# Performance work log

Measured on AMD Instinct MI355X. Metric: run time of the kernel, lower is better.

Reference implementation:

```python
import jax, jax.numpy as jnp
import numpy as np

N, E, H, ED, S = 20000, 320000, 256, 64, 4  # nodes, edges, hidden, edge_dim, message_steps


def setup_inputs() -> dict:
    key = jax.random.key(0)
    ks = jax.random.split(key, 20)
    w = lambda k, shape: jax.random.normal(k, shape, dtype=jnp.float32) * 0.02
    inp = {
        "node_state": jax.random.normal(ks[0], (N, H), dtype=jnp.float32),
        "edge_attr": jax.random.normal(ks[1], (E, ED), dtype=jnp.float32),
        # per-step stacked parameters (S steps)
        "nn_g": jnp.ones((S, H), jnp.float32),  # node_norm gamma
        "nn_b": jnp.zeros((S, H), jnp.float32),
        "mn_g": jnp.ones((S, H), jnp.float32),  # msg_norm gamma
        "mn_b": jnp.zeros((S, H), jnp.float32),
        "eW1": w(ks[2], (S, 2 * H + ED, H)), "eb1": jnp.zeros((S, H), jnp.float32),
        "eW2": w(ks[3], (S, H, H)),          "eb2": jnp.zeros((S, H), jnp.float32),
        "nW1": w(ks[4], (S, 2 * H, 2 * H)),  "nb1": jnp.zeros((S, 2 * H), jnp.float32),
        "nW2": w(ks[5], (S, 2 * H, H)),      "nb2": jnp.zeros((S, H), jnp.float32),
        "edge_index": jax.random.randint(ks[6], (2, E), 0, N, dtype=jnp.int64),
    }
    return inp


def _layer_norm(x, g, b, eps=1e-5):
    m = jnp.mean(x, axis=-1, keepdims=True)
    v = jnp.var(x, axis=-1, keepdims=True)
    return (x - m) * jax.lax.rsqrt(v + eps) * g + b


def reference(node_state, edge_attr, nn_g, nn_b, mn_g, mn_b,
              eW1, eb1, eW2, eb2, nW1, nb1, nW2, nb2, edge_index):
    n = node_state.shape[0]
    src, dst = edge_index[0], edge_index[1]
    ones = jnp.ones((dst.shape[0], 1), node_state.dtype)
    deg = jax.ops.segment_sum(ones, dst, num_segments=n)  # [N,1], same each step
    deg = jnp.maximum(deg, 1.0)
    h = node_state
    for i in range(nn_g.shape[0]):  # fixed small number of message steps
        hn = _layer_norm(h, nn_g[i], nn_b[i])                       # [N,H]
        x = jnp.concatenate([hn[src], hn[dst], edge_attr], axis=1)  # [E,2H+ED]
        msg = jax.nn.silu(x @ eW1[i] + eb1[i]) @ eW2[i] + eb2[i]    # [E,H]
        agg = jax.ops.segment_sum(msg, dst, num_segments=n)         # [N,H]
        agg = _layer_norm(agg / deg, mn_g[i], mn_b[i])
        y = jnp.concatenate([hn, agg], axis=1)                      # [N,2H]
        h = h + (jax.nn.silu(y @ nW1[i] + nb1[i]) @ nW2[i] + nb2[i])
    return h
```

## Files before the change

### kernel.cpp

```cpp
#include <hip/hip_runtime.h>
#include <hip/hip_bf16.h>
#include <stdint.h>

#define NN 20000
#define NE 320000
#define HH 256
#define EDK 64
#define NSTEPS 4
#define ECH 160000
#define NCHUNK 2
#define WSTEP 606208

typedef __attribute__((ext_vector_type(8))) short bf16x8;
typedef __attribute__((ext_vector_type(4))) float f32x4;

__device__ __forceinline__ float silu_f(float x) { return x / (1.0f + __expf(-x)); }

__device__ __forceinline__ unsigned short f2bf(float f) {
    __hip_bfloat16 h = __float2bfloat16(f);
    return __builtin_bit_cast(unsigned short, h);
}
__device__ __forceinline__ float bf2f(unsigned short u) {
    unsigned int x = ((unsigned int)u) << 16;
    return __builtin_bit_cast(float, x);
}
__device__ __forceinline__ unsigned int pk2(float a, float b) {
    return (unsigned int)f2bf(a) | ((unsigned int)f2bf(b) << 16);
}

__global__ void ln_kernel(const float* __restrict__ x, const float* __restrict__ g,
                          const float* __restrict__ b, float* __restrict__ y, int M)
{
    int row  = blockIdx.x * 4 + (threadIdx.x >> 6);
    int lane = threadIdx.x & 63;
    if (row >= M) return;
    float4 v = *(const float4*)(x + (size_t)row * HH + lane * 4);
    float s  = v.x + v.y + v.z + v.w;
    float ss = v.x*v.x + v.y*v.y + v.z*v.z + v.w*v.w;
#pragma unroll
    for (int off = 32; off > 0; off >>= 1) {
        s  += __shfl_down(s, off);
        ss += __shfl_down(ss, off);
    }
    float mean = __shfl(s, 0) * (1.0f / HH);
    float ms   = __shfl(ss, 0) * (1.0f / HH);
    float rstd = rsqrtf(ms - mean * mean + 1e-5f);
    float4 gg = *(const float4*)(g + lane * 4);
    float4 bb = *(const float4*)(b + lane * 4);
    float4 o;
    o.x = (v.x - mean) * rstd * gg.x + bb.x;
    o.y = (v.y - mean) * rstd * gg.y + bb.y;
    o.z = (v.z - mean) * rstd * gg.z + bb.z;
    o.w = (v.w - mean) * rstd * gg.w + bb.w;
    *(float4*)(y + (size_t)row * HH + lane * 4) = o;
}

__global__ void wtr_kernel(const float* __restrict__ eW1, const float* __restrict__ eW2,
                           const float* __restrict__ nW1, const float* __restrict__ nW2,
                           unsigned short* __restrict__ wbuf)
{
    int bx = blockIdx.x;
    int s  = bx / 592, t = bx % 592;
    const float* e1 = eW1 + (size_t)s * 576 * 256;
    unsigned short* wb = wbuf + (size_t)s * WSTEP;
    const float* src; unsigned short* dst; int K, N;
    if      (t < 64)  { src = e1;                          K = 256; N = 256; dst = wb; }
    else if (t < 128) { src = e1 + 65536;                  K = 256; N = 256; dst = wb + 65536;  t -= 64; }
    else if (t < 144) { src = e1 + 131072;                 K = 64;  N = 256; dst = wb + 131072; t -= 128; }
    else if (t < 208) { src = eW2 + (size_t)s * 65536;     K = 256; N = 256; dst = wb + 147456; t -= 144; }
    else if (t < 464) { src = nW1 + (size_t)s * 262144;    K = 512; N = 512; dst = wb + 212992; t -= 208; }
    else              { src = nW2 + (size_t)s * 131072;    K = 512; N = 256; dst = wb + 475136; t -= 464; }
    int ntn = N >> 5;
    int tk = t / ntn, tn = t % ntn;
    int k0 = tk * 32, n0 = tn * 32;
    __shared__ float ts[32][33];
    int tx = threadIdx.x & 31, ty = threadIdx.x >> 5;
#pragma unroll
    for (int i = 0; i < 4; i++)
        ts[ty + i * 8][tx] = src[(size_t)(k0 + ty + i * 8) * N + n0 + tx];
    __syncthreads();
#pragma unroll
    for (int i = 0; i < 4; i++)
        dst[(size_t)(n0 + ty + i * 8) * K + k0 + tx] = f2bf(ts[tx][ty + i * 8]);
}

#define GBM 128
#define GBN 128
#define GBK 64
template <int EPI, int ASRC, bool BF16OUT>
__global__ __launch_bounds__(256) void mgemm(
    const float* __restrict__ A, const float* __restrict__ A2, int lda,
    const unsigned short* __restrict__ BT,
    const float* __restrict__ bias, const int* __restrict__ cnt,
    const int* __restrict__ Aidx, int rowoff,
    void* __restrict__ Cout, int M, int Nc, int K)
{
    __shared__ unsigned short lsA[GBM * GBK];
    __shared__ unsigned short lsB[GBN * GBK];
    const int tid = threadIdx.x;
    const int row0 = blockIdx.x * GBM, col0 = blockIdx.y * GBN;
    const int r = tid >> 1, half = tid & 1;
    const int w = tid >> 6, l = tid & 63;
    const int wm = w >> 1, wn = w & 1;

    int grow = row0 + r;
    bool aval = (grow < M);
    const float* arow = nullptr;
    if (ASRC == 1) { if (aval) arow = A + (size_t)Aidx[rowoff + grow] * lda; }
    else if (ASRC == 0) { if (aval) arow = A + (size_t)grow * lda; }
    const unsigned short* brow = BT + (size_t)(col0 + r) * K;

    f32x4 acc[4][4] = {};

    for (int k0 = 0; k0 < K; k0 += GBK) {
        {
            const float* ap = nullptr;
            if (ASRC == 2) {
                if (aval) ap = ((k0 < 256) ? A : A2) + (size_t)grow * 256 + (k0 & 255) + half * 32;
            } else {
                if (aval) ap = arow + k0 + half * 32;
            }
            float4 fv[8];
            if (ap) {
#pragma unroll
                for (int i = 0; i < 8; i++) fv[i] = ((const float4*)ap)[i];
            } else {
#pragma unroll
                for (int i = 0; i < 8; i++) fv[i] = make_float4(0.f, 0.f, 0.f, 0.f);
            }
#pragma unroll
            for (int ci = 0; ci < 4; ci++) {
                uint4 q;
                q.x = pk2(fv[2*ci].x,   fv[2*ci].y);
                q.y = pk2(fv[2*ci].z,   fv[2*ci].w);
                q.z = pk2(fv[2*ci+1].x, fv[2*ci+1].y);
                q.w = pk2(fv[2*ci+1].z, fv[2*ci+1].w);
                int slot = half * 4 + ci;
                int phys = slot ^ (r & 7);
                *(uint4*)&lsA[r * GBK + phys * 8] = q;
            }
        }
        {
            const unsigned short* bp = brow + k0 + half * 32;
#pragma unroll
            for (int ci = 0; ci < 4; ci++) {
                uint4 q = ((const uint4*)bp)[ci];
                int slot = half * 4 + ci;
                int phys = slot ^ (r & 7);
                *(uint4*)&lsB[r * GBK + phys * 8] = q;
            }
        }
        __syncthreads();
#pragma unroll
        for (int ks = 0; ks < 2; ks++) {
            bf16x8 bfr[4];
#pragma unroll
            for (int n = 0; n < 4; n++) {
                int rn = wn * 64 + n * 16 + (l & 15);
                int phys = (ks * 4 + (l >> 4)) ^ (rn & 7);
                bfr[n] = *(bf16x8*)&lsB[rn * GBK + phys * 8];
            }
#pragma unroll
            for (int m = 0; m < 4; m++) {
                int rm = wm * 64 + m * 16 + (l & 15);
                int phys = (ks * 4 + (l >> 4)) ^ (rm & 7);
                bf16x8 af = *(bf16x8*)&lsA[rm * GBK + phys * 8];
#pragma unroll
                for (int n = 0; n < 4; n++)
                    acc[m][n] = __builtin_amdgcn_mfma_f32_16x16x32_bf16(af, bfr[n], acc[m][n], 0, 0, 0);
            }
        }
        __syncthreads();
    }

    float* Cf = (float*)Cout;
    unsigned short* Cb = (unsigned short*)Cout;
    const int cbase = col0 + wn * 64 + (l & 15);
#pragma unroll
    for (int n = 0; n < 4; n++) {
        int c = cbase + n * 16;
        float bv = bias ? bias[c] : 0.0f;
#pragma unroll
        for (int m = 0; m < 4; m++) {
            int rbase = row0 + wm * 64 + m * 16 + (l >> 4) * 4;
#pragma unroll
            for (int i = 0; i < 4; i++) {
                int rr = rbase + i;
                if (rr >= M) continue;
                float o = acc[m][n][i];
                if (EPI == 2) {
                    float cf = (float)cnt[rr];
                    o = (o + cf * bv) / fmaxf(cf, 1.0f);
                } else {
                    o += bv;
                    if (EPI == 1) o = silu_f(o);
                }
                size_t off = (size_t)rr * Nc + c;
                if (EPI == 3)       { Cf[off] += o; }
                else if (BF16OUT)   { Cb[off] = f2bf(o); }
                else                { Cf[off] = o; }
            }
        }
    }
}

__global__ void agg_kernel(const unsigned short* __restrict__ Pa, const unsigned short* __restrict__ Pb,
                           const unsigned short* __restrict__ Pe, const int* __restrict__ esrc,
                           const int* __restrict__ rowptr,
                           float* __restrict__ u, int e0, int e1)
{
    int node = blockIdx.x * 4 + (threadIdx.x >> 6);
    if (node >= NN) return;
    int beg = rowptr[node], end = rowptr[node + 1];
    int lo = beg > e0 ? beg : e0;
    int hi = end < e1 ? end : e1;
    if (lo >= hi) return;
    int lane = threadIdx.x & 63;
    int j = lane * 4;
    ushort4 pb4 = *(const ushort4*)(Pb + (size_t)node * HH + j);
    float b0 = bf2f(pb4.x), b1 = bf2f(pb4.y), b2 = bf2f(pb4.z), b3 = bf2f(pb4.w);
    float a0 = 0.f, a1 = 0.f, a2 = 0.f, a3 = 0.f;
    for (int p = lo; p < hi; ++p) {
        int src = esrc[p];
        ushort4 pa4 = *(const ushort4*)(Pa + (size_t)src * HH + j);
        ushort4 pe4 = *(const ushort4*)(Pe + (size_t)(p - e0) * HH + j);
        a0 += silu_f(bf2f(pa4.x) + b0 + bf2f(pe4.x));
        a1 += silu_f(bf2f(pa4.y) + b1 + bf2f(pe4.y));
        a2 += silu_f(bf2f(pa4.z) + b2 + bf2f(pe4.z));
        a3 += silu_f(bf2f(pa4.w) + b3 + bf2f(pe4.w));
    }
    float* up = u + (size_t)node * HH + j;
    float4 uo = *(const float4*)up;
    uo.x += a0; uo.y += a1; uo.z += a2; uo.w += a3;
    *(float4*)up = uo;
}

__global__ void detect_kernel(const uint32_t* __restrict__ w, int* flag)
{
    int i = blockIdx.x * 256 + threadIdx.x;
    bool bad = false;
    if (i < NE) {
        uint32_t lo = w[2 * i], hi = w[2 * i + 1];
        bad = (hi != 0u) || (lo >= (uint32_t)NN);
    }
    if (__any(bad)) {
        if ((threadIdx.x & 63) == 0) atomicAnd(flag, 0);
    }
}
__global__ void convert_kernel(const uint32_t* __restrict__ w, const int* __restrict__ flag,
                               int* __restrict__ out)
{
    int i = blockIdx.x * 256 + threadIdx.x;
    if (i >= 2 * NE) return;
    out[i] = (*flag) ? (int)w[2 * i] : (int)w[i];
}
__global__ void deg_kernel(const int* __restrict__ idx, int* __restrict__ cnt)
{
    int e = blockIdx.x * 256 + threadIdx.x;
    if (e < NE) atomicAdd(cnt + idx[NE + e], 1);
}

__global__ void scan_kernel(const int* __restrict__ cnt, int* __restrict__ rowptr)
{
    __shared__ int part[1024];
    const int T = 1024, PER = (NN + T - 1) / T;
    int t = threadIdx.x;
    int base = t * PER;
    int s = 0;
    for (int i = 0; i < PER; i++) {
        int idx = base + i;
        if (idx < NN) s += cnt[idx];
    }
    part[t] = s;
    __syncthreads();
    for (int off = 1; off < T; off <<= 1) {
        int v = (t >= off) ? part[t - off] : 0;
        __syncthreads();
        part[t] += v;
        __syncthreads();
    }
    int run = (t == 0) ? 0 : part[t - 1];
    for (int i = 0; i < PER; i++) {
        int idx = base + i;
        if (idx < NN) { rowptr[idx] = run; run += cnt[idx]; }
    }
    if (t == T - 1) rowptr[NN] = part[T - 1];
}

__global__ void fill_kernel(const int* __restrict__ idx, const int* __restrict__ rowptr,
                            int* __restrict__ fillc, int* __restrict__ esrc,
                            int* __restrict__ eorig)
{
    int e = blockIdx.x * 256 + threadIdx.x;
    if (e >= NE) return;
    int dst = idx[NE + e];
    int pos = rowptr[dst] + atomicAdd(fillc + dst, 1);
    esrc[pos]  = idx[e];
    eorig[pos] = e;
}

extern "C" void kernel_launch(void* const* d_in, const int* in_sizes, int n_in,
                              void* d_out, int out_size, void* d_ws, size_t ws_size,
                              hipStream_t stream)
{
    const float* node_state = (const float*)d_in[0];
    const float* edge_attr  = (const float*)d_in[1];
    const float* nn_g = (const float*)d_in[2];
    const float* nn_b = (const float*)d_in[3];
    const float* mn_g = (const float*)d_in[4];
    const float* mn_b = (const float*)d_in[5];
    const float* eW1  = (const float*)d_in[6];
    const float* eb1  = (const float*)d_in[7];
    const float* eW2  = (const float*)d_in[8];
    const float* eb2  = (const float*)d_in[9];
    const float* nW1  = (const float*)d_in[10];
    const float* nb1  = (const float*)d_in[11];
    const float* nW2  = (const float*)d_in[12];
    const float* nb2  = (const float*)d_in[13];
    const uint32_t* eidx_raw = (const uint32_t*)d_in[14];

    const size_t SZ = (size_t)NN * HH;
    const size_t BIGBYTES = (size_t)ECH * HH * 2;
    float* ws   = (float*)d_ws;
    float* hn   = ws;
    float* u    = hn + SZ;
    float* aggb = u + SZ;
    unsigned short* Pa = (unsigned short*)(aggb + SZ);
    unsigned short* Pb = Pa + SZ;
    char* bigc  = (char*)(Pb + SZ);
    unsigned short* Pe = (unsigned short*)bigc;
    float* z    = (float*)bigc;
    unsigned short* wbuf = (unsigned short*)(bigc + BIGBYTES);
    int* idx32  = (int*)(wbuf + 4 * WSTEP);
    int* esrc   = idx32 + 2 * NE;
    int* eorig  = esrc + NE;
    int* rowptr = eorig + NE;
    int* cnt    = rowptr + NN + 1;
    int* fillc  = cnt + NN;
    int* flag   = fillc + NN;
    size_t needed = ((size_t)(flag + 1) - (size_t)d_ws);
    if (ws_size < needed) return;

    float* h = (float*)d_out;

    hipMemcpyAsync(h, node_state, SZ * sizeof(float), hipMemcpyDeviceToDevice, stream);

    wtr_kernel<<<4 * 592, 256, 0, stream>>>(eW1, eW2, nW1, nW2, wbuf);
    hipMemsetAsync(flag, 0xFF, sizeof(int), stream);
    detect_kernel<<<(NE + 255) / 256, 256, 0, stream>>>(eidx_raw, flag);
    convert_kernel<<<(2 * NE + 255) / 256, 256, 0, stream>>>(eidx_raw, flag, idx32);
    hipMemsetAsync(cnt, 0, NN * sizeof(int), stream);
    deg_kernel<<<(NE + 255) / 256, 256, 0, stream>>>(idx32, cnt);
    scan_kernel<<<1, 1024, 0, stream>>>(cnt, rowptr);
    hipMemsetAsync(fillc, 0, NN * sizeof(int), stream);
    fill_kernel<<<(NE + 255) / 256, 256, 0, stream>>>(idx32, rowptr, fillc, esrc, eorig);

    const dim3 gN2((NN + GBM - 1) / GBM, 2);
    const dim3 gN4((NN + GBM - 1) / GBM, 4);
    const dim3 gPe(ECH / GBM, 2);

    for (int s = 0; s < NSTEPS; s++) {
        const unsigned short* wb = wbuf + (size_t)s * WSTEP;
        const unsigned short* WaT   = wb;
        const unsigned short* WbT   = wb + 65536;
        const unsigned short* WcT   = wb + 131072;
        const unsigned short* eW2T  = wb + 147456;
        const unsigned short* nW1T  = wb + 212992;
        const unsigned short* nW2T  = wb + 475136;
        const float* eb1s = eb1 + (size_t)s * HH;
        const float* eb2s = eb2 + (size_t)s * HH;
        const float* nb1s = nb1 + (size_t)s * 512;
        const float* nb2s = nb2 + (size_t)s * HH;

        ln_kernel<<<NN / 4, 256, 0, stream>>>(h, nn_g + s * HH, nn_b + s * HH, hn, NN);
        mgemm<0, 0, true><<<gN2, 256, 0, stream>>>(hn, nullptr, HH, WaT, nullptr, nullptr, nullptr, 0, Pa, NN, HH, HH);
        mgemm<0, 0, true><<<gN2, 256, 0, stream>>>(hn, nullptr, HH, WbT, nullptr, nullptr, nullptr, 0, Pb, NN, HH, HH);
        hipMemsetAsync(u, 0, SZ * sizeof(float), stream);
        for (int c = 0; c < NCHUNK; c++) {
            int e0 = c * ECH, e1 = e0 + ECH;
            mgemm<0, 1, true><<<gPe, 256, 0, stream>>>(edge_attr, nullptr, EDK, WcT, eb1s, nullptr, eorig, e0, Pe, ECH, HH, EDK);
            agg_kernel<<<(NN + 3) / 4, 256, 0, stream>>>(Pa, Pb, Pe, esrc, rowptr, u, e0, e1);
        }
        mgemm<2, 0, false><<<gN2, 256, 0, stream>>>(u, nullptr, HH, eW2T, eb2s, cnt, nullptr, 0, aggb, NN, HH, HH);
        ln_kernel<<<NN / 4, 256, 0, stream>>>(aggb, mn_g + s * HH, mn_b + s * HH, aggb, NN);
        mgemm<1, 2, false><<<gN4, 256, 0, stream>>>(hn, aggb, HH, nW1T, nb1s, nullptr, nullptr, 0, z, NN, 512, 512);
        mgemm<3, 0, false><<<gN2, 256, 0, stream>>>(z, nullptr, 512, nW2T, nb2s, nullptr, nullptr, 0, h, NN, HH, 512);
    }
}
```

Before: 1.896 ms.

## Presort edge attributes to bf16, merge Pa/Pb GEMM, bf16 intermediates, LDS-staged stores

Edge attributes are gathered once into destination-sorted bf16 order, so the per-step edge GEMM reads contiguous bf16 rows instead of gathering fp32 through an index. The two node projections run as one GEMM with N=512 into an interleaved Pab buffer. The nW1 output z is stored as bf16 and read directly by the nW2 GEMM. bf16 GEMM outputs are staged through swizzled LDS for coalesced 16-byte stores, agg_kernel prefetches the next source index, and the edge chunk size is halved to make room for the new buffers. The changes cut memory traffic and launches, at the cost of an extra bf16 rounding on z and more chunk launches.

```diff
diff --git a/kernel.cpp b/kernel.cpp
--- a/kernel.cpp
+++ b/kernel.cpp
@@ -7,8 +7,8 @@
 #define HH 256
 #define EDK 64
 #define NSTEPS 4
-#define ECH 160000
-#define NCHUNK 2
+#define ECH 80000
+#define NCHUNK 4
 #define WSTEP 606208
 
 typedef __attribute__((ext_vector_type(8))) short bf16x8;
@@ -84,41 +84,65 @@
         dst[(size_t)(n0 + ty + i * 8) * K + k0 + tx] = f2bf(ts[tx][ty + i * 8]);
 }
 
+__global__ void easort_kernel(const float* __restrict__ ea, const int* __restrict__ eorig,
+                              unsigned short* __restrict__ out)
+{
+    int gid = blockIdx.x * 256 + threadIdx.x;
+    int p = gid >> 4, q = gid & 15;
+    if (p >= NE) return;
+    float4 v = *(const float4*)(ea + (size_t)eorig[p] * EDK + q * 4);
+    ushort4 o;
+    o.x = f2bf(v.x); o.y = f2bf(v.y); o.z = f2bf(v.z); o.w = f2bf(v.w);
+    *(ushort4*)(out + (size_t)p * EDK + q * 4) = o;
+}
+
 #define GBM 128
 #define GBN 128
 #define GBK 64
 template <int EPI, int ASRC, bool BF16OUT>
 __global__ __launch_bounds__(256) void mgemm(
-    const float* __restrict__ A, const float* __restrict__ A2, int lda,
+    const void* __restrict__ A, const float* __restrict__ A2, int lda,
     const unsigned short* __restrict__ BT,
     const float* __restrict__ bias, const int* __restrict__ cnt,
-    const int* __restrict__ Aidx, int rowoff,
     void* __restrict__ Cout, int M, int Nc, int K)
 {
-    __shared__ unsigned short lsA[GBM * GBK];
-    __shared__ unsigned short lsB[GBN * GBK];
+    __shared__ unsigned short smem[GBM * GBK + GBN * GBK];
+    unsigned short* lsA = smem;
+    unsigned short* lsB = smem + GBM * GBK;
     const int tid = threadIdx.x;
     const int row0 = blockIdx.x * GBM, col0 = blockIdx.y * GBN;
     const int r = tid >> 1, half = tid & 1;
     const int w = tid >> 6, l = tid & 63;
     const int wm = w >> 1, wn = w & 1;
 
+    const float* Af = (const float*)A;
+    const unsigned short* Ab = (const unsigned short*)A;
     int grow = row0 + r;
     bool aval = (grow < M);
-    const float* arow = nullptr;
-    if (ASRC == 1) { if (aval) arow = A + (size_t)Aidx[rowoff + grow] * lda; }
-    else if (ASRC == 0) { if (aval) arow = A + (size_t)grow * lda; }
     const unsigned short* brow = BT + (size_t)(col0 + r) * K;
 
     f32x4 acc[4][4] = {};
 
     for (int k0 = 0; k0 < K; k0 += GBK) {
-        {
+        if constexpr (ASRC == 3) {
+            uint4 q[4] = {};
+            if (aval) {
+                const unsigned short* ap = Ab + (size_t)grow * lda + k0 + half * 32;
+#pragma unroll
+                for (int ci = 0; ci < 4; ci++) q[ci] = ((const uint4*)ap)[ci];
+            }
+#pragma unroll
+            for (int ci = 0; ci < 4; ci++) {
+                int slot = half * 4 + ci;
+                int phys = slot ^ (r & 7);
+                *(uint4*)&lsA[r * GBK + phys * 8] = q[ci];
+            }
+        } else {
             const float* ap = nullptr;
-            if (ASRC == 2) {
-                if (aval) ap = ((k0 < 256) ? A : A2) + (size_t)grow * 256 + (k0 & 255) + half * 32;
+            if constexpr (ASRC == 2) {
+                if (aval) ap = ((k0 < 256) ? Af : A2) + (size_t)grow * 256 + (k0 & 255) + half * 32;
             } else {
-                if (aval) ap = arow + k0 + half * 32;
+                if (aval) ap = Af + (size_t)grow * lda + k0 + half * 32;
             }
             float4 fv[8];
             if (ap) {
@@ -173,38 +197,71 @@
         __syncthreads();
     }
 
-    float* Cf = (float*)Cout;
-    unsigned short* Cb = (unsigned short*)Cout;
-    const int cbase = col0 + wn * 64 + (l & 15);
-#pragma unroll
-    for (int n = 0; n < 4; n++) {
-        int c = cbase + n * 16;
-        float bv = bias ? bias[c] : 0.0f;
-#pragma unroll
-        for (int m = 0; m < 4; m++) {
-            int rbase = row0 + wm * 64 + m * 16 + (l >> 4) * 4;
-#pragma unroll
-            for (int i = 0; i < 4; i++) {
-                int rr = rbase + i;
-                if (rr >= M) continue;
-                float o = acc[m][n][i];
-                if (EPI == 2) {
-                    float cf = (float)cnt[rr];
-                    o = (o + cf * bv) / fmaxf(cf, 1.0f);
-                } else {
-                    o += bv;
+    if constexpr (BF16OUT) {
+        unsigned short* Cb = (unsigned short*)Cout;
+#pragma unroll
+        for (int n = 0; n < 4; n++) {
+            int cl = wn * 64 + n * 16 + (l & 15);
+            float bv = bias ? bias[col0 + cl] : 0.0f;
+#pragma unroll
+            for (int m = 0; m < 4; m++) {
+                int rbase = wm * 64 + m * 16 + (l >> 4) * 4;
+#pragma unroll
+                for (int i = 0; i < 4; i++) {
+                    int rl = rbase + i;
+                    float o = acc[m][n][i] + bv;
                     if (EPI == 1) o = silu_f(o);
+                    int chunk = cl >> 3;
+                    int phys = chunk ^ (rl & 15);
+                    smem[rl * 128 + phys * 8 + (cl & 7)] = f2bf(o);
                 }
-                size_t off = (size_t)rr * Nc + c;
-                if (EPI == 3)       { Cf[off] += o; }
-                else if (BF16OUT)   { Cb[off] = f2bf(o); }
-                else                { Cf[off] = o; }
-            }
-        }
-    }
-}
-
-__global__ void agg_kernel(const unsigned short* __restrict__ Pa, const unsigned short* __restrict__ Pb,
+            }
+        }
+        __syncthreads();
+        int orow = tid >> 1, hf = tid & 1;
+        int rr = row0 + orow;
+        if (rr < M) {
+            unsigned short* crow = Cb + (size_t)rr * Nc + col0;
+#pragma unroll
+            for (int c8 = 0; c8 < 8; c8++) {
+                int chunk = hf * 8 + c8;
+                int phys = chunk ^ (orow & 15);
+                uint4 v = *(uint4*)&smem[orow * 128 + phys * 8];
+                *(uint4*)(crow + chunk * 8) = v;
+            }
+        }
+    } else {
+        float* Cf = (float*)Cout;
+        const int cbase = col0 + wn * 64 + (l & 15);
+#pragma unroll
+        for (int n = 0; n < 4; n++) {
+            int c = cbase + n * 16;
+            float bv = bias ? bias[c] : 0.0f;
+#pragma unroll
+            for (int m = 0; m < 4; m++) {
+                int rbase = row0 + wm * 64 + m * 16 + (l >> 4) * 4;
+#pragma unroll
+                for (int i = 0; i < 4; i++) {
+                    int rr = rbase + i;
+                    if (rr >= M) continue;
+                    float o = acc[m][n][i];
+                    if (EPI == 2) {
+                        float cf = (float)cnt[rr];
+                        o = (o + cf * bv) / fmaxf(cf, 1.0f);
+                    } else {
+                        o += bv;
+                        if (EPI == 1) o = silu_f(o);
+                    }
+                    size_t off = (size_t)rr * Nc + c;
+                    if (EPI == 3) Cf[off] += o;
+                    else          Cf[off] = o;
+                }
+            }
+        }
+    }
+}
+
+__global__ void agg_kernel(const unsigned short* __restrict__ Pab,
                            const unsigned short* __restrict__ Pe, const int* __restrict__ esrc,
                            const int* __restrict__ rowptr,
                            float* __restrict__ u, int e0, int e1)
@@ -217,12 +274,14 @@
     if (lo >= hi) return;
     int lane = threadIdx.x & 63;
     int j = lane * 4;
-    ushort4 pb4 = *(const ushort4*)(Pb + (size_t)node * HH + j);
+    ushort4 pb4 = *(const ushort4*)(Pab + (size_t)node * 512 + 256 + j);
     float b0 = bf2f(pb4.x), b1 = bf2f(pb4.y), b2 = bf2f(pb4.z), b3 = bf2f(pb4.w);
     float a0 = 0.f, a1 = 0.f, a2 = 0.f, a3 = 0.f;
+    int src_n = esrc[lo];
     for (int p = lo; p < hi; ++p) {
-        int src = esrc[p];
-        ushort4 pa4 = *(const ushort4*)(Pa + (size_t)src * HH + j);
+        int src = src_n;
+        if (p + 1 < hi) src_n = esrc[p + 1];
+        ushort4 pa4 = *(const ushort4*)(Pab + (size_t)src * 512 + j);
         ushort4 pe4 = *(const ushort4*)(Pe + (size_t)(p - e0) * HH + j);
         a0 += silu_f(bf2f(pa4.x) + b0 + bf2f(pe4.x));
         a1 += silu_f(bf2f(pa4.y) + b1 + bf2f(pe4.y));
@@ -320,17 +379,14 @@
     const uint32_t* eidx_raw = (const uint32_t*)d_in[14];
 
     const size_t SZ = (size_t)NN * HH;
-    const size_t BIGBYTES = (size_t)ECH * HH * 2;
-    float* ws   = (float*)d_ws;
-    float* hn   = ws;
-    float* u    = hn + SZ;
-    float* aggb = u + SZ;
-    unsigned short* Pa = (unsigned short*)(aggb + SZ);
-    unsigned short* Pb = Pa + SZ;
-    char* bigc  = (char*)(Pb + SZ);
-    unsigned short* Pe = (unsigned short*)bigc;
-    float* z    = (float*)bigc;
-    unsigned short* wbuf = (unsigned short*)(bigc + BIGBYTES);
+    float* hn = (float*)d_ws;
+    float* u  = hn + SZ;
+    unsigned short* Pab = (unsigned short*)(u + SZ);
+    unsigned short* eas = Pab + (size_t)NN * 512;
+    unsigned short* Pe  = eas + (size_t)NE * EDK;
+    float* aggb = (float*)Pe;
+    unsigned short* zb = (unsigned short*)((char*)Pe + (size_t)NN * HH * 4);
+    unsigned short* wbuf = Pe + (size_t)ECH * HH;
     int* idx32  = (int*)(wbuf + 4 * WSTEP);
     int* esrc   = idx32 + 2 * NE;
     int* eorig  = esrc + NE;
@@ -354,6 +410,7 @@
     scan_kernel<<<1, 1024, 0, stream>>>(cnt, rowptr);
     hipMemsetAsync(fillc, 0, NN * sizeof(int), stream);
     fill_kernel<<<(NE + 255) / 256, 256, 0, stream>>>(idx32, rowptr, fillc, esrc, eorig);
+    easort_kernel<<<(NE * 16) / 256, 256, 0, stream>>>(edge_attr, eorig, eas);
 
     const dim3 gN2((NN + GBM - 1) / GBM, 2);
     const dim3 gN4((NN + GBM - 1) / GBM, 4);
@@ -361,29 +418,27 @@
 
     for (int s = 0; s < NSTEPS; s++) {
         const unsigned short* wb = wbuf + (size_t)s * WSTEP;
-        const unsigned short* WaT   = wb;
-        const unsigned short* WbT   = wb + 65536;
-        const unsigned short* WcT   = wb + 131072;
-        const unsigned short* eW2T  = wb + 147456;
-        const unsigned short* nW1T  = wb + 212992;
-        const unsigned short* nW2T  = wb + 475136;
+        const unsigned short* WabT = wb;
+        const unsigned short* WcT  = wb + 131072;
+        const unsigned short* eW2T = wb + 147456;
+        const unsigned short* nW1T = wb + 212992;
+        const unsigned short* nW2T = wb + 475136;
         const float* eb1s = eb1 + (size_t)s * HH;
         const float* eb2s = eb2 + (size_t)s * HH;
         const float* nb1s = nb1 + (size_t)s * 512;
         const float* nb2s = nb2 + (size_t)s * HH;
 
         ln_kernel<<<NN / 4, 256, 0, stream>>>(h, nn_g + s * HH, nn_b + s * HH, hn, NN);
-        mgemm<0, 0, true><<<gN2, 256, 0, stream>>>(hn, nullptr, HH, WaT, nullptr, nullptr, nullptr, 0, Pa, NN, HH, HH);
-        mgemm<0, 0, true><<<gN2, 256, 0, stream>>>(hn, nullptr, HH, WbT, nullptr, nullptr, nullptr, 0, Pb, NN, HH, HH);
+        mgemm<0, 0, true><<<gN4, 256, 0, stream>>>(hn, nullptr, HH, WabT, nullptr, nullptr, Pab, NN, 512, HH);
         hipMemsetAsync(u, 0, SZ * sizeof(float), stream);
         for (int c = 0; c < NCHUNK; c++) {
             int e0 = c * ECH, e1 = e0 + ECH;
-            mgemm<0, 1, true><<<gPe, 256, 0, stream>>>(edge_attr, nullptr, EDK, WcT, eb1s, nullptr, eorig, e0, Pe, ECH, HH, EDK);
-            agg_kernel<<<(NN + 3) / 4, 256, 0, stream>>>(Pa, Pb, Pe, esrc, rowptr, u, e0, e1);
-        }
-        mgemm<2, 0, false><<<gN2, 256, 0, stream>>>(u, nullptr, HH, eW2T, eb2s, cnt, nullptr, 0, aggb, NN, HH, HH);
+            mgemm<0, 3, true><<<gPe, 256, 0, stream>>>(eas + (size_t)e0 * EDK, nullptr, EDK, WcT, eb1s, nullptr, Pe, ECH, HH, EDK);
+            agg_kernel<<<(NN + 3) / 4, 256, 0, stream>>>(Pab, Pe, esrc, rowptr, u, e0, e1);
+        }
+        mgemm<2, 0, false><<<gN2, 256, 0, stream>>>(u, nullptr, HH, eW2T, eb2s, cnt, aggb, NN, HH, HH);
         ln_kernel<<<NN / 4, 256, 0, stream>>>(aggb, mn_g + s * HH, mn_b + s * HH, aggb, NN);
-        mgemm<1, 2, false><<<gN4, 256, 0, stream>>>(hn, aggb, HH, nW1T, nb1s, nullptr, nullptr, 0, z, NN, 512, 512);
-        mgemm<3, 0, false><<<gN2, 256, 0, stream>>>(z, nullptr, 512, nW2T, nb2s, nullptr, nullptr, 0, h, NN, HH, 512);
-    }
-}
+        mgemm<1, 2, true><<<gN4, 256, 0, stream>>>(hn, aggb, HH, nW1T, nb1s, nullptr, zb, NN, 512, 512);
+        mgemm<3, 3, false><<<gN2, 256, 0, stream>>>(zb, nullptr, 512, nW2T, nb2s, nullptr, h, NN, HH, 512);
+    }
+}
```

Measured after the change: 1.855 ms. -2.2%, faster.
